# Kernel optimization log

Measured on AMD Instinct MI355X. Metric: run time of the kernel, lower is better.

The kernel has to match this reference:

```python
import jax, jax.numpy as jnp
import numpy as np

N_EMBD = 1024
N_HEAD = 16
HEAD_DIM = N_EMBD // N_HEAD


def setup_inputs() -> dict:
    key = jax.random.key(0)
    ks = jax.random.split(key, 9)
    B, T, C = 2, 2048, N_EMBD
    s = 1.0 / np.sqrt(C)
    x = jax.random.normal(ks[0], (B, T, C), dtype=jnp.float32)
    Wk = jax.random.normal(ks[1], (C, C), dtype=jnp.float32) * s
    bk = jnp.zeros((C,), dtype=jnp.float32)
    Wq = jax.random.normal(ks[2], (C, C), dtype=jnp.float32) * s
    bq = jnp.zeros((C,), dtype=jnp.float32)
    Wv = jax.random.normal(ks[3], (C, C), dtype=jnp.float32) * s
    bv = jnp.zeros((C,), dtype=jnp.float32)
    Wp = jax.random.normal(ks[4], (C, C), dtype=jnp.float32) * s
    bp = jnp.zeros((C,), dtype=jnp.float32)
    return {"x": x, "Wk": Wk, "bk": bk, "Wq": Wq, "bq": bq,
            "Wv": Wv, "bv": bv, "Wp": Wp, "bp": bp}


def reference(x, Wk, bk, Wq, bq, Wv, bv, Wp, bp):
    B, T, C = x.shape
    H, D = N_HEAD, HEAD_DIM
    # torch Linear: y = x @ W.T + b
    k = (x @ Wk.T + bk).reshape(B, T, H, D)  # [B,T,H,D]
    q = (x @ Wq.T + bq).reshape(B, T, H, D)
    v = (x @ Wv.T + bv).reshape(B, T, H, D)
    scale = 1.0 / jnp.sqrt(jnp.asarray(D, dtype=x.dtype))
    scores = jnp.einsum('bqhd,bkhd->bhqk', q, k) * scale  # [B,H,T,T]
    w = jax.nn.softmax(scores, axis=-1)
    attn = jnp.einsum('bhqk,bkhd->bqhd', w, v).reshape(B, T, C)
    return attn @ Wp.T + bp
```

## Files before the change

### kernel.cpp

```cpp
#include <hip/hip_runtime.h>
#include <hip/hip_bf16.h>
#include <stdint.h>

#define TT 2048
#define CC 1024
#define NH 16
#define HD 64
#define QKVN 3072

typedef __attribute__((ext_vector_type(8))) short short8;
typedef __attribute__((ext_vector_type(4))) float floatx4;
typedef __attribute__((ext_vector_type(4))) unsigned short ushortx4;

typedef const __attribute__((address_space(1))) void gas_void;
typedef __attribute__((address_space(3))) void las_void;

__device__ __forceinline__ void gload16(const void* g, void* l) {
  __builtin_amdgcn_global_load_lds((gas_void*)g, (las_void*)l, 16, 0, 0);
}

__device__ __forceinline__ unsigned short f2bf(float f) {
  union { float f; uint32_t u; } v; v.f = f;
  uint32_t u = v.u;
  uint32_t r = (u + 0x7fffu + ((u >> 16) & 1u)) >> 16;
  return (unsigned short)r;
}

__device__ __forceinline__ float fexp2(float x) {
#if __has_builtin(__builtin_amdgcn_exp2f)
  return __builtin_amdgcn_exp2f(x);
#else
  return exp2f(x);
#endif
}

#define QSCALE 0.18033688011112042f

__device__ __forceinline__ int perm64(int t) {
  const int kk = t >> 5, r5 = t & 31;
  const int g = ((r5 >> 3) & 2) | ((r5 >> 2) & 1);
  const int slot = (r5 & 3) | ((r5 >> 1) & 4);
  return kk * 32 + g * 8 + slot;
}

__global__ __launch_bounds__(256) void cvt_fused(const float* __restrict__ x,
                                                 const float* __restrict__ wq,
                                                 const float* __restrict__ wk,
                                                 const float* __restrict__ wv,
                                                 const float* __restrict__ wp,
                                                 unsigned short* __restrict__ xb,
                                                 unsigned short* __restrict__ wqkvb,
                                                 unsigned short* __restrict__ wpb) {
  const int i = blockIdx.x * blockDim.x + threadIdx.x;
  if (i < 1048576) {
    const float4 v = reinterpret_cast<const float4*>(x)[i];
    ushortx4 o; o[0] = f2bf(v.x); o[1] = f2bf(v.y); o[2] = f2bf(v.z); o[3] = f2bf(v.w);
    reinterpret_cast<ushortx4*>(xb)[i] = o;
    return;
  }
  const int j = i - 1048576;
  const int seg = j >> 18;
  const int idx = j & 262143;
  const float* src = (seg == 0) ? wq : (seg == 1) ? wk : (seg == 2) ? wv : wp;
  const float sc = (seg == 0) ? QSCALE : 1.0f;
  const float4 v = reinterpret_cast<const float4*>(src)[idx];
  ushortx4 o;
  o[0] = f2bf(v.x * sc); o[1] = f2bf(v.y * sc); o[2] = f2bf(v.z * sc); o[3] = f2bf(v.w * sc);
  if (seg < 3)
    reinterpret_cast<ushortx4*>(wqkvb)[j] = o;
  else
    reinterpret_cast<ushortx4*>(wpb)[idx] = o;
}

__global__ __launch_bounds__(512) void gemm_qkv(const unsigned short* __restrict__ A,
                                                const unsigned short* __restrict__ W,
                                                const float* __restrict__ b0,
                                                const float* __restrict__ b1,
                                                const float* __restrict__ b2,
                                                unsigned short* __restrict__ out,
                                                unsigned short* __restrict__ Vt) {
  __shared__ unsigned short lsA[2][256 * 64];
  __shared__ unsigned short lsB[2][192 * 64];
  const int tid = threadIdx.x;
  const int wave = tid >> 6, lane = tid & 63;
  const int g = lane >> 4, c16 = lane & 15;
  const int orig = blockIdx.x;
  const int vid = (orig & 7) * 32 + (orig >> 3);
  const int chk = vid >> 5, wrm = vid & 31;
  const int m0 = ((chk & 3) * 4 + (wrm & 3)) * 256;
  const int n0 = ((chk >> 2) * 8 + (wrm >> 2)) * 192;
  const int wm = (wave >> 2) * 128, wn = (wave & 3) * 48;

  floatx4 acc[8][3];
#pragma unroll
  for (int i = 0; i < 8; ++i)
#pragma unroll
    for (int j = 0; j < 3; ++j) acc[i][j] = (floatx4){0.f, 0.f, 0.f, 0.f};

  const int srow = lane >> 3, sj = lane & 7;
  const int gj = (sj ^ srow) << 3;

  const unsigned short* aSrc = A + (size_t)(m0 + wave * 32 + srow) * CC + gj;
  const unsigned short* bSrc = W + (size_t)(n0 + wave * 24 + srow) * CC + gj;

  auto stageT = [&](int buf) {
    char* la = (char*)lsA[buf] + (wave * 4) * 1024;
    char* lb = (char*)lsB[buf] + (wave * 3) * 1024;
#pragma unroll
    for (int rho = 0; rho < 4; ++rho)
      gload16(aSrc + (size_t)rho * 8 * CC, la + rho * 1024);
#pragma unroll
    for (int rho = 0; rho < 3; ++rho)
      gload16(bSrc + (size_t)rho * 8 * CC, lb + rho * 1024);
    aSrc += 64;
    bSrc += 64;
  };

  stageT(0);
  stageT(1);
  asm volatile("s_waitcnt vmcnt(7)" ::: "memory");
  __builtin_amdgcn_s_barrier();

#pragma unroll 2
  for (int t = 0; t < 16; ++t) {
    const int buf = t & 1;
    const char* la = (const char*)lsA[buf];
    const char* lb = (const char*)lsB[buf];
    short8 af[8][2], bfr[3][2];
#pragma unroll
    for (int i = 0; i < 8; ++i) {
      const int ra = wm + i * 16 + c16;
#pragma unroll
      for (int kk = 0; kk < 2; ++kk) {
        const int ca = (kk * 4 + g) ^ (ra & 7);
        af[i][kk] = *reinterpret_cast<const short8*>(la + ra * 128 + (ca << 4));
      }
    }
#pragma unroll
    for (int j = 0; j < 3; ++j) {
      const int rb = wn + j * 16 + c16;
#pragma unroll
      for (int kk = 0; kk < 2; ++kk) {
        const int cb = (kk * 4 + g) ^ (rb & 7);
        bfr[j][kk] = *reinterpret_cast<const short8*>(lb + rb * 128 + (cb << 4));
      }
    }
    __builtin_amdgcn_s_setprio(1);
#pragma unroll
    for (int kk = 0; kk < 2; ++kk)
#pragma unroll
      for (int i = 0; i < 8; ++i)
#pragma unroll
        for (int j = 0; j < 3; ++j)
          acc[i][j] = __builtin_amdgcn_mfma_f32_16x16x32_bf16(af[i][kk], bfr[j][kk],
                                                              acc[i][j], 0, 0, 0);
    __builtin_amdgcn_s_setprio(0);
    if (t < 15) {
      __builtin_amdgcn_s_barrier();
      if (t < 14) {
        stageT(buf);
        asm volatile("s_waitcnt vmcnt(7)" ::: "memory");
      } else {
        asm volatile("s_waitcnt vmcnt(0)" ::: "memory");
      }
      __builtin_amdgcn_s_barrier();
    }
  }

  const int rgrp = g * 4;
#pragma unroll
  for (int i = 0; i < 8; ++i) {
    const int tk0 = m0 + wm + i * 16 + rgrp;
    const int bb = tk0 >> 11;
    const int tw = tk0 & 2047;
    const int tpos = (tw & ~63) + perm64(tw & 63);
#pragma unroll
    for (int j = 0; j < 3; ++j) {
      const int gn = n0 + wn + j * 16 + c16;
      const int seg = gn >> 10;
      const float bv = ((seg == 0) ? b0 : (seg == 1) ? b1 : b2)[gn & 1023] *
                       ((seg == 0) ? QSCALE : 1.0f);
      if (gn >= 2048) {
        const int vdim = gn - 2048;
        const int h = vdim >> 6, d = vdim & 63;
        ushortx4 ov;
#pragma unroll
        for (int r = 0; r < 4; ++r) ov[r] = f2bf(acc[i][j][r] + bv);
        *reinterpret_cast<ushortx4*>(
            &Vt[((size_t)((bb * NH + h) * HD + d)) * TT + tpos]) = ov;
      } else {
#pragma unroll
        for (int r = 0; r < 4; ++r)
          out[(size_t)(tk0 + r) * QKVN + gn] = f2bf(acc[i][j][r] + bv);
      }
    }
  }
}

__global__ __launch_bounds__(256) void gemm_proj(const unsigned short* __restrict__ A,
                                                 const unsigned short* __restrict__ W,
                                                 const float* __restrict__ bias,
                                                 float* __restrict__ outv) {
  __shared__ unsigned short lsA[2][128 * 64];
  __shared__ unsigned short lsB[2][128 * 64];
  const int tid = threadIdx.x;
  const int wave = tid >> 6, lane = tid & 63;
  const int orig = blockIdx.x;
  const int vid = (orig & 7) * 32 + (orig >> 3);
  const int chk = vid >> 5, wrm = vid & 31;
  const int m0 = ((chk & 3) * 8 + (wrm >> 2)) * 128;
  const int n0 = ((chk >> 2) * 4 + (wrm & 3)) * 128;
  const int wm = (wave >> 1) * 64, wn = (wave & 1) * 64;
  const int K = CC, N = CC;

  floatx4 acc[4][4];
#pragma unroll
  for (int i = 0; i < 4; ++i)
#pragma unroll
    for (int j = 0; j < 4; ++j)
      acc[i][j] = (floatx4){0.f, 0.f, 0.f, 0.f};

  const int sr = lane >> 3;
  const int sj = lane & 7;
  const int gj = (sj ^ sr) << 3;

  const unsigned short* aSrc = A + (size_t)(m0 + wave * 32 + sr) * K + gj;
  const unsigned short* bSrc = W + (size_t)(n0 + wave * 32 + sr) * K + gj;

  auto stageT = [&](int buf) {
    char* la = (char*)lsA[buf] + (wave * 4) * 1024;
    char* lb = (char*)lsB[buf] + (wave * 4) * 1024;
#pragma unroll
    for (int t = 0; t < 4; ++t) {
      gload16(aSrc + (size_t)t * 8 * K, la + t * 1024);
      gload16(bSrc + (size_t)t * 8 * K, lb + t * 1024);
    }
    aSrc += 64;
    bSrc += 64;
  };

  stageT(0);
  stageT(1);
  asm volatile("s_waitcnt vmcnt(8)" ::: "memory");
  __builtin_amdgcn_s_barrier();

#pragma unroll 2
  for (int t = 0; t < 16; ++t) {
    const int buf = t & 1;
    const char* la = (const char*)lsA[buf];
    const char* lb = (const char*)lsB[buf];
    short8 af[4][2], bfr[4][2];
#pragma unroll
    for (int i = 0; i < 4; ++i) {
      const int ra = wm + i * 16 + (lane & 15);
      const int rb = wn + i * 16 + (lane & 15);
#pragma unroll
      for (int kk = 0; kk < 2; ++kk) {
        const int ca = (kk * 4 + (lane >> 4)) ^ (ra & 7);
        const int cb = (kk * 4 + (lane >> 4)) ^ (rb & 7);
        af[i][kk] = *reinterpret_cast<const short8*>(la + ra * 128 + (ca << 4));
        bfr[i][kk] = *reinterpret_cast<const short8*>(lb + rb * 128 + (cb << 4));
      }
    }
    __builtin_amdgcn_s_setprio(1);
#pragma unroll
    for (int kk = 0; kk < 2; ++kk)
#pragma unroll
      for (int i = 0; i < 4; ++i)
#pragma unroll
        for (int j = 0; j < 4; ++j)
          acc[i][j] = __builtin_amdgcn_mfma_f32_16x16x32_bf16(af[i][kk], bfr[j][kk],
                                                              acc[i][j], 0, 0, 0);
    __builtin_amdgcn_s_setprio(0);
    if (t < 15) {
      __builtin_amdgcn_s_barrier();
      if (t < 14) {
        stageT(buf);
        asm volatile("s_waitcnt vmcnt(8)" ::: "memory");
      } else {
        asm volatile("s_waitcnt vmcnt(0)" ::: "memory");
      }
      __builtin_amdgcn_s_barrier();
    }
  }

  const int col = lane & 15;
  const int rgrp = (lane >> 4) * 4;
#pragma unroll
  for (int i = 0; i < 4; ++i) {
    const int gm0 = m0 + wm + i * 16 + rgrp;
#pragma unroll
    for (int j = 0; j < 4; ++j) {
      const int gn = n0 + wn + j * 16 + col;
      const float bv = bias[gn];
#pragma unroll
      for (int r = 0; r < 4; ++r)
        outv[(size_t)(gm0 + r) * N + gn] = acc[i][j][r] + bv;
    }
  }
}

__global__ __launch_bounds__(256) void attn_fwd(const unsigned short* __restrict__ QKV,
                                                const unsigned short* __restrict__ Vt,
                                                unsigned short* __restrict__ Ob) {
  __shared__ unsigned short lsK[3][64 * 64];
  __shared__ unsigned short lsV[2][64 * 64];
  const int tid = threadIdx.x;
  const int wave = tid >> 6, lane = tid & 63;
  const int g = lane >> 4;
  const int c16 = lane & 15;
  const int bh = blockIdx.x;
  const int b = bh >> 4, h = bh & 15;
  const int q0 = blockIdx.y * 64 + wave * 16;

  short8 qf[2];
  {
    const unsigned short* qp =
        QKV + (size_t)(b * TT + q0 + c16) * QKVN + h * HD + g * 8;
    qf[0] = *reinterpret_cast<const short8*>(qp);
    qf[1] = *reinterpret_cast<const short8*>(qp + 32);
  }

  short8 ones;
#pragma unroll
  for (int i = 0; i < 8; ++i) ones[i] = (short)0x3F80;

  floatx4 o[4];
#pragma unroll
  for (int f = 0; f < 4; ++f) o[f] = (floatx4){0.f, 0.f, 0.f, 0.f};
  floatx4 lacc = (floatx4){0.f, 0.f, 0.f, 0.f};

  const int sr = lane >> 3, sj = lane & 7;
  const int gj = (sj ^ sr) << 3;

  const unsigned short* kSrc =
      QKV + (size_t)(b * TT + wave * 16 + sr) * QKVN + CC + h * HD + gj;
  const unsigned short* vSrc = Vt + ((size_t)bh * HD + wave * 16 + sr) * TT + gj;

  auto stageK = [&](int buf) {
    char* lk = (char*)lsK[buf] + (wave * 2) * 1024;
    gload16(kSrc, lk);
    gload16(kSrc + (size_t)8 * QKVN, lk + 1024);
    kSrc += (size_t)64 * QKVN;
  };
  auto stageV = [&](int buf) {
    char* lv = (char*)lsV[buf] + (wave * 2) * 1024;
    gload16(vSrc, lv);
    gload16(vSrc + (size_t)8 * TT, lv + 1024);
    vSrc += 64;
  };

  auto compute = [&](const unsigned short* lk, const unsigned short* lv) {
    floatx4 s[4];
#pragma unroll
    for (int cb = 0; cb < 4; ++cb) s[cb] = (floatx4){0.f, 0.f, 0.f, 0.f};
    __builtin_amdgcn_s_setprio(1);
#pragma unroll
    for (int kk = 0; kk < 2; ++kk) {
#pragma unroll
      for (int cb = 0; cb < 4; ++cb) {
        const int rk = cb * 16 + c16;
        const int ck = (kk * 4 + g) ^ (rk & 7);
        const short8 kf =
            *reinterpret_cast<const short8*>((const char*)lk + rk * 128 + (ck << 4));
        s[cb] = __builtin_amdgcn_mfma_f32_16x16x32_bf16(kf, qf[kk], s[cb], 0, 0, 0);
      }
    }
    __builtin_amdgcn_s_setprio(0);

    unsigned int w[4][2];
#pragma unroll
    for (int cb = 0; cb < 4; ++cb) {
#pragma unroll
      for (int r = 0; r < 4; ++r) s[cb][r] = fexp2(s[cb][r]);
      asm("v_cvt_pk_bf16_f32 %0, %1, %2"
          : "=v"(w[cb][0]) : "v"(s[cb][0]), "v"(s[cb][1]));
      asm("v_cvt_pk_bf16_f32 %0, %1, %2"
          : "=v"(w[cb][1]) : "v"(s[cb][2]), "v"(s[cb][3]));
    }

#pragma unroll
    for (int kk = 0; kk < 2; ++kk) {
      unsigned int pa0 = w[2 * kk][0], pb0 = w[2 * kk + 1][0];
      unsigned int pa1 = w[2 * kk][1], pb1 = w[2 * kk + 1][1];
      asm("v_permlane32_swap_b32 %0, %1" : "+v"(pa0), "+v"(pb0));
      asm("v_permlane32_swap_b32 %0, %1" : "+v"(pa1), "+v"(pb1));
      union { unsigned int u[4]; short8 v; } pk;
      pk.u[0] = pa0; pk.u[1] = pa1; pk.u[2] = pb0; pk.u[3] = pb1;
      const short8 pbv = pk.v;
      __builtin_amdgcn_s_setprio(1);
#pragma unroll
      for (int f = 0; f < 4; ++f) {
        const int rv = f * 16 + c16;
        const int cv = (4 * kk + g) ^ (rv & 7);
        const short8 vf =
            *reinterpret_cast<const short8*>((const char*)lv + rv * 128 + (cv << 4));
        o[f] = __builtin_amdgcn_mfma_f32_16x16x32_bf16(vf, pbv, o[f], 0, 0, 0);
      }
      lacc = __builtin_amdgcn_mfma_f32_16x16x32_bf16(ones, pbv, lacc, 0, 0, 0);
      __builtin_amdgcn_s_setprio(0);
    }
  };

  stageV(0);
  stageK(0);
  stageK(1);

#pragma unroll 2
  for (int it = 0; it < TT / 64; ++it) {
    if (it < TT / 64 - 1)
      asm volatile("s_waitcnt vmcnt(2)" ::: "memory");
    else
      asm volatile("s_waitcnt vmcnt(0)" ::: "memory");
    __builtin_amdgcn_s_barrier();
    if (it + 1 < TT / 64) stageV((it + 1) & 1);
    if (it + 2 < TT / 64) stageK((it + 2) % 3);
    compute((const unsigned short*)lsK[it % 3], (const unsigned short*)lsV[it & 1]);
  }

  {
    const float inv = 1.0f / lacc[0];
    const size_t gm = (size_t)(b * TT + q0 + c16) * CC;
#pragma unroll
    for (int f = 0; f < 4; ++f) {
      ushortx4 ov;
#pragma unroll
      for (int r = 0; r < 4; ++r) ov[r] = f2bf(o[f][r] * inv);
      *reinterpret_cast<ushortx4*>(&Ob[gm + h * HD + f * 16 + 4 * g]) = ov;
    }
  }
}

extern "C" void kernel_launch(void* const* d_in, const int* in_sizes, int n_in,
                              void* d_out, int out_size, void* d_ws, size_t ws_size,
                              hipStream_t stream) {
  (void)in_sizes; (void)n_in; (void)out_size; (void)ws_size;
  const float* x  = (const float*)d_in[0];
  const float* Wk = (const float*)d_in[1];
  const float* bk = (const float*)d_in[2];
  const float* Wq = (const float*)d_in[3];
  const float* bq = (const float*)d_in[4];
  const float* Wv = (const float*)d_in[5];
  const float* bv = (const float*)d_in[6];
  const float* Wp = (const float*)d_in[7];
  const float* bp = (const float*)d_in[8];
  float* out = (float*)d_out;

  char* ws = (char*)d_ws;
  const size_t MB = 1u << 20;
  unsigned short* xb    = (unsigned short*)(ws);
  unsigned short* Wqkvb = (unsigned short*)(ws + 8 * MB);
  unsigned short* Wpb   = (unsigned short*)(ws + 14 * MB);
  unsigned short* QKVb  = (unsigned short*)(ws + 16 * MB);
  unsigned short* Vtb   = (unsigned short*)(ws + 40 * MB);
  unsigned short* Ab    = (unsigned short*)(ws + 48 * MB);

  cvt_fused<<<8192, 256, 0, stream>>>(x, Wq, Wk, Wv, Wp, xb, Wqkvb, Wpb);

  gemm_qkv<<<256, 512, 0, stream>>>(xb, Wqkvb, bq, bk, bv, QKVb, Vtb);

  attn_fwd<<<dim3(2 * NH, TT / 64), 256, 0, stream>>>(QKVb, Vtb, Ab);

  gemm_proj<<<256, 256, 0, stream>>>(Ab, Wpb, bp, out);
}
```

Baseline: 116.3 us.

## Triple-buffer LDS tiles in QKV and projection GEMMs with one barrier per step

Both GEMM kernels move from a double-buffered K loop with two barriers per iteration to a triple-buffered (A-only in the QKV kernel, A and B in the projection kernel) pipeline. Loads are issued two tiles ahead, and there is a single waitcnt+barrier at the top of each iteration. This aims to hide global-to-LDS latency better and cut barrier stalls. In exchange it uses more LDS per block: the QKV kernel grows to about 144KB, which may limit occupancy or approach the LDS limit. Buffer indexing now uses modulo 3, and the unroll-2 pragma is dropped.

```diff
diff --git a/kernel.cpp b/kernel.cpp
--- a/kernel.cpp
+++ b/kernel.cpp
@@ -79,7 +79,7 @@
                                                 const float* __restrict__ b2,
                                                 unsigned short* __restrict__ out,
                                                 unsigned short* __restrict__ Vt) {
-  __shared__ unsigned short lsA[2][256 * 64];
+  __shared__ unsigned short lsA[3][256 * 64];
   __shared__ unsigned short lsB[2][192 * 64];
   const int tid = threadIdx.x;
   const int wave = tid >> 6, lane = tid & 63;
@@ -103,29 +103,36 @@
   const unsigned short* aSrc = A + (size_t)(m0 + wave * 32 + srow) * CC + gj;
   const unsigned short* bSrc = W + (size_t)(n0 + wave * 24 + srow) * CC + gj;
 
-  auto stageT = [&](int buf) {
+  auto stageA = [&](int buf) {
     char* la = (char*)lsA[buf] + (wave * 4) * 1024;
-    char* lb = (char*)lsB[buf] + (wave * 3) * 1024;
 #pragma unroll
     for (int rho = 0; rho < 4; ++rho)
       gload16(aSrc + (size_t)rho * 8 * CC, la + rho * 1024);
+    aSrc += 64;
+  };
+  auto stageB = [&](int buf) {
+    char* lb = (char*)lsB[buf] + (wave * 3) * 1024;
 #pragma unroll
     for (int rho = 0; rho < 3; ++rho)
       gload16(bSrc + (size_t)rho * 8 * CC, lb + rho * 1024);
-    aSrc += 64;
     bSrc += 64;
   };
 
-  stageT(0);
-  stageT(1);
-  asm volatile("s_waitcnt vmcnt(7)" ::: "memory");
-  __builtin_amdgcn_s_barrier();
-
-#pragma unroll 2
+  stageB(0);
+  stageA(0);
+  stageA(1);
+
   for (int t = 0; t < 16; ++t) {
-    const int buf = t & 1;
-    const char* la = (const char*)lsA[buf];
-    const char* lb = (const char*)lsB[buf];
+    if (t < 15)
+      asm volatile("s_waitcnt vmcnt(4)" ::: "memory");
+    else
+      asm volatile("s_waitcnt vmcnt(0)" ::: "memory");
+    __builtin_amdgcn_s_barrier();
+    if (t + 1 < 16) stageB((t + 1) & 1);
+    if (t + 2 < 16) stageA((t + 2) % 3);
+
+    const char* la = (const char*)lsA[t % 3];
+    const char* lb = (const char*)lsB[t & 1];
     short8 af[8][2], bfr[3][2];
 #pragma unroll
     for (int i = 0; i < 8; ++i) {
@@ -155,16 +162,6 @@
           acc[i][j] = __builtin_amdgcn_mfma_f32_16x16x32_bf16(af[i][kk], bfr[j][kk],
                                                               acc[i][j], 0, 0, 0);
     __builtin_amdgcn_s_setprio(0);
-    if (t < 15) {
-      __builtin_amdgcn_s_barrier();
-      if (t < 14) {
-        stageT(buf);
-        asm volatile("s_waitcnt vmcnt(7)" ::: "memory");
-      } else {
-        asm volatile("s_waitcnt vmcnt(0)" ::: "memory");
-      }
-      __builtin_amdgcn_s_barrier();
-    }
   }
 
   const int rgrp = g * 4;
@@ -201,8 +198,8 @@
                                                  const unsigned short* __restrict__ W,
                                                  const float* __restrict__ bias,
                                                  float* __restrict__ outv) {
-  __shared__ unsigned short lsA[2][128 * 64];
-  __shared__ unsigned short lsB[2][128 * 64];
+  __shared__ unsigned short lsA[3][128 * 64];
+  __shared__ unsigned short lsB[3][128 * 64];
   const int tid = threadIdx.x;
   const int wave = tid >> 6, lane = tid & 63;
   const int orig = blockIdx.x;
@@ -241,14 +238,17 @@
 
   stageT(0);
   stageT(1);
-  asm volatile("s_waitcnt vmcnt(8)" ::: "memory");
-  __builtin_amdgcn_s_barrier();
-
-#pragma unroll 2
+
   for (int t = 0; t < 16; ++t) {
-    const int buf = t & 1;
-    const char* la = (const char*)lsA[buf];
-    const char* lb = (const char*)lsB[buf];
+    if (t < 15)
+      asm volatile("s_waitcnt vmcnt(8)" ::: "memory");
+    else
+      asm volatile("s_waitcnt vmcnt(0)" ::: "memory");
+    __builtin_amdgcn_s_barrier();
+    if (t + 2 < 16) stageT((t + 2) % 3);
+
+    const char* la = (const char*)lsA[t % 3];
+    const char* lb = (const char*)lsB[t % 3];
     short8 af[4][2], bfr[4][2];
 #pragma unroll
     for (int i = 0; i < 4; ++i) {
@@ -272,16 +272,6 @@
           acc[i][j] = __builtin_amdgcn_mfma_f32_16x16x32_bf16(af[i][kk], bfr[j][kk],
                                                               acc[i][j], 0, 0, 0);
     __builtin_amdgcn_s_setprio(0);
-    if (t < 15) {
-      __builtin_amdgcn_s_barrier();
-      if (t < 14) {
-        stageT(buf);
-        asm volatile("s_waitcnt vmcnt(8)" ::: "memory");
-      } else {
-        asm volatile("s_waitcnt vmcnt(0)" ::: "memory");
-      }
-      __builtin_amdgcn_s_barrier();
-    }
   }
 
   const int col = lane & 15;
```

Measured after the change: 117.6 us. Within noise of the previous version (+1.1%).
